# Kernel tuning notes

Hardware: AMD Instinct MI355X
Metric: run time of the kernel (lower is better)

Reference implementation:

```python
import jax, jax.numpy as jnp
import numpy as np

N_NODES = 50000
N_EDGES = 600000
IN_DIM = 128
HID = 128
OUT_DIM = 2
N_GRAPHS = 64
EPS = 1e-12  # F.normalize default eps


def setup_inputs() -> dict:
    key = jax.random.key(0)
    ks = jax.random.split(key, 16)
    s = 0.05
    x = jax.random.normal(ks[0], (N_NODES, IN_DIM), jnp.float32)
    edge_index = jax.random.randint(ks[1], (2, N_EDGES), 0, N_NODES, dtype=jnp.int32)
    batch = jnp.sort(jax.random.randint(ks[2], (N_NODES,), 0, N_GRAPHS, dtype=jnp.int32))
    # GraphSage layer 0: lin (IN->HID), agg_lin (IN+HID -> HID)
    lin_w0 = jax.random.normal(ks[3], (IN_DIM, HID), jnp.float32) * s
    lin_b0 = jnp.zeros((HID,), jnp.float32)
    agg_w0 = jax.random.normal(ks[4], (HID + IN_DIM, HID), jnp.float32) * s
    agg_b0 = jnp.zeros((HID,), jnp.float32)
    # GraphSage layer 1: lin (HID->HID), agg_lin (2*HID -> HID)
    lin_w1 = jax.random.normal(ks[5], (HID, HID), jnp.float32) * s
    lin_b1 = jnp.zeros((HID,), jnp.float32)
    agg_w1 = jax.random.normal(ks[6], (2 * HID, HID), jnp.float32) * s
    agg_b1 = jnp.zeros((HID,), jnp.float32)
    # post_mp: Linear(HID,HID) -> Dropout -> Linear(HID,OUT)
    mp_w1 = jax.random.normal(ks[7], (HID, HID), jnp.float32) * s
    mp_b1 = jnp.zeros((HID,), jnp.float32)
    mp_w2 = jax.random.normal(ks[8], (HID, OUT_DIM), jnp.float32) * s
    mp_b2 = jnp.zeros((OUT_DIM,), jnp.float32)
    return dict(x=x, edge_index=edge_index, batch=batch,
                lin_w0=lin_w0, lin_b0=lin_b0, agg_w0=agg_w0, agg_b0=agg_b0,
                lin_w1=lin_w1, lin_b1=lin_b1, agg_w1=agg_w1, agg_b1=agg_b1,
                mp_w1=mp_w1, mp_b1=mp_b1, mp_w2=mp_w2, mp_b2=mp_b2)


def sage_layer(x, lin_w, lin_b, agg_w, agg_b, src, dst, num_nodes):
    # message: ReLU(Linear(x_j)) gathered along source nodes  [E, HID]
    msg = jax.nn.relu(x[src] @ lin_w + lin_b)
    # aggr='mean' scatter to target nodes
    summed = jax.ops.segment_sum(msg, dst, num_segments=num_nodes)
    deg = jax.ops.segment_sum(jnp.ones((src.shape[0], 1), x.dtype), dst,
                              num_segments=num_nodes)
    agg = summed / jnp.maximum(deg, 1.0)
    # update: ReLU(Linear([aggr, x])) then L2-normalize rows
    h = jax.nn.relu(jnp.concatenate([agg, x], axis=-1) @ agg_w + agg_b)
    norm = jnp.sqrt(jnp.sum(h * h, axis=1, keepdims=True))
    return h / jnp.maximum(norm, EPS)


def reference(x, edge_index, batch,
              lin_w0, lin_b0, agg_w0, agg_b0,
              lin_w1, lin_b1, agg_w1, agg_b1,
              mp_w1, mp_b1, mp_w2, mp_b2):
    src, dst = edge_index[0], edge_index[1]
    n = x.shape[0]
    h = sage_layer(x, lin_w0, lin_b0, agg_w0, agg_b0, src, dst, n)
    # F.relu is a no-op on the non-negative normalized output; dropout p=0 -> identity
    h = sage_layer(h, lin_w1, lin_b1, agg_w1, agg_b1, src, dst, n)
    # global max pool over graphs
    pooled = jax.ops.segment_max(h, batch, num_segments=N_GRAPHS)
    pooled = jnp.where(jnp.isfinite(pooled), pooled, 0.0)  # guard empty graphs
    # post_mp: Linear -> Dropout(identity) -> Linear
    z = (pooled @ mp_w1 + mp_b1) @ mp_w2 + mp_b2
    return jax.nn.log_softmax(z, axis=1)
```

## Files before the change

### kernel.cpp

```cpp
#include <hip/hip_runtime.h>

__device__ __forceinline__ float bf2f(ushort u) {
    union { uint i; float f; } c; c.i = ((uint)u) << 16; return c.f;
}
__device__ __forceinline__ float bf2lo(uint v) {
    union { uint i; float f; } c; c.i = v << 16; return c.f;
}
__device__ __forceinline__ float bf2hi(uint v) {
    union { uint i; float f; } c; c.i = v & 0xffff0000u; return c.f;
}
__device__ __forceinline__ ushort f2bf(float f) {
    union { float f; uint i; } c; c.f = f;
    uint b = c.i;
    uint r = (b + 0x7fffu + ((b >> 16) & 1u)) >> 16;
    return (ushort)r;
}

typedef __bf16 v8bf __attribute__((ext_vector_type(8)));
typedef float  v4f  __attribute__((ext_vector_type(4)));

__device__ __forceinline__ ushort load_conv(const void* src, int i, int isf32) {
    return isf32 ? f2bf(((const float*)src)[i]) : ((const ushort*)src)[i];
}

struct SmallSrcs { const void* p[8]; };
__global__ __launch_bounds__(256) void phaseA(
    const void* __restrict__ x, ushort* __restrict__ xb, int nx, int nbconv,
    const void* __restrict__ w0, const void* __restrict__ wa0,
    const void* __restrict__ w1, const void* __restrict__ wa1,
    ushort* __restrict__ t0, ushort* __restrict__ ta0,
    ushort* __restrict__ t1, ushort* __restrict__ ta1,
    SmallSrcs s, ushort* __restrict__ smalldst,
    int* __restrict__ deg, int* __restrict__ pooled, int N, int G,
    int* __restrict__ flagOut) {
    __shared__ int sred[256];
    int b = blockIdx.x, t = threadIdx.x;
    {
        const uint* words = (const uint*)x;
        int bad = 0;
        for (int i = t; i < 2048; i += 256) {
            uint w = words[i];
            uint exp = (w >> 7) & 0xffu;
            if (exp >= 143u) bad++;
        }
        sred[t] = bad;
        __syncthreads();
        for (int o = 128; o; o >>= 1) {
            if (t < o) sred[t] += sred[t + o];
            __syncthreads();
        }
    }
    const int isf = sred[0] > 64 ? 1 : 0;
    if (b == 0 && t == 0) *flagOut = isf;

    if (b < nbconv) {
        int idx = b * 256 + t;
        int base = idx * 8;
        if (base + 8 <= nx) {
            if (isf) {
                const float4* s4 = (const float4*)x;
                float4 a = s4[idx * 2], bb = s4[idx * 2 + 1];
                union { ushort u[8]; uint4 v; } o;
                o.u[0] = f2bf(a.x); o.u[1] = f2bf(a.y); o.u[2] = f2bf(a.z); o.u[3] = f2bf(a.w);
                o.u[4] = f2bf(bb.x); o.u[5] = f2bf(bb.y); o.u[6] = f2bf(bb.z); o.u[7] = f2bf(bb.w);
                *(uint4*)(xb + base) = o.v;
            } else {
                *(uint4*)(xb + base) = ((const uint4*)x)[idx];
            }
        } else {
            for (int i = base; i < nx; i++) xb[i] = load_conv(x, i, isf);
        }
    } else if (b < nbconv + 452) {
        int idx = (b - nbconv) * 256 + t;
        if (idx < 98304) {
            const void* W; ushort* T; int K; int local;
            if (idx < 16384)      { W = w0;  T = t0;  K = 128; local = idx; }
            else if (idx < 49152) { W = wa0; T = ta0; K = 256; local = idx - 16384; }
            else if (idx < 65536) { W = w1;  T = t1;  K = 128; local = idx - 49152; }
            else                  { W = wa1; T = ta1; K = 256; local = idx - 65536; }
            ushort v = load_conv(W, local, isf);
            int k = local >> 7;
            int n = local & 127;
            T[(size_t)n * K + k] = v;
        } else {
            int si = idx - 98304;
            if (si < 17282) {
                const int offs[9] = {0, 128, 256, 384, 512, 16896, 17024, 17280, 17282};
                int seg = 0;
                while (si >= offs[seg + 1]) seg++;
                smalldst[si] = load_conv(s.p[seg], si - offs[seg], isf);
            }
        }
    } else {
        int idx = (b - nbconv - 452) * 256 + t;
        int nd4 = N >> 2;
        int4 z = {0, 0, 0, 0};
        if (idx < nd4) ((int4*)deg)[idx] = z;
        else if (idx == nd4) { for (int i = nd4 * 4; i < N; i++) deg[i] = 0; }
        else if (idx - nd4 - 1 < G * 32) ((int4*)pooled)[idx - nd4 - 1] = z;
    }
}

__global__ __launch_bounds__(256) void count_deg(const int* __restrict__ dst, int* __restrict__ deg, int E) {
    int i = blockIdx.x * 256 + threadIdx.x;
    if (i < E) atomicAdd(&deg[dst[i]], 1);
}

#define SCAN_CHUNK 1024

__global__ __launch_bounds__(256) void chunk_sum_kernel(const int* __restrict__ deg,
                                                        int* __restrict__ csums, int n) {
    __shared__ int s[256];
    int t = threadIdx.x;
    int base = blockIdx.x * SCAN_CHUNK + t * 4;
    int v = 0;
    if (base + 4 <= n) {
        int4 q = *(const int4*)(deg + base);
        v = q.x + q.y + q.z + q.w;
    } else {
        for (int i = base; i < n; i++) v += deg[i];
    }
    s[t] = v;
    __syncthreads();
    for (int o = 128; o; o >>= 1) {
        if (t < o) s[t] += s[t + o];
        __syncthreads();
    }
    if (t == 0) csums[blockIdx.x] = s[0];
}

__global__ __launch_bounds__(256) void scan_phase2(const int* __restrict__ deg,
                                                   const int* __restrict__ csums,
                                                   int* __restrict__ rowptr, int* __restrict__ cursor,
                                                   int n) {
    __shared__ int red[256];
    int t = threadIdx.x, b = blockIdx.x;
    int v = 0;
    for (int i = t; i < b; i += 256) v += csums[i];
    red[t] = v;
    __syncthreads();
    for (int o = 128; o; o >>= 1) {
        if (t < o) red[t] += red[t + o];
        __syncthreads();
    }
    int chunkOff = red[0];
    __syncthreads();
    int base = b * SCAN_CHUNK + t * 4;
    int d0 = 0, d1 = 0, d2 = 0, d3 = 0;
    if (base + 4 <= n) {
        int4 q = *(const int4*)(deg + base);
        d0 = q.x; d1 = q.y; d2 = q.z; d3 = q.w;
    } else {
        if (base < n)     d0 = deg[base];
        if (base + 1 < n) d1 = deg[base + 1];
        if (base + 2 < n) d2 = deg[base + 2];
        if (base + 3 < n) d3 = deg[base + 3];
    }
    int s4 = d0 + d1 + d2 + d3;
    red[t] = s4;
    __syncthreads();
    for (int o = 1; o < 256; o <<= 1) {
        int u = (t >= o) ? red[t - o] : 0;
        __syncthreads();
        red[t] += u;
        __syncthreads();
    }
    int run = chunkOff + red[t] - s4;
    if (base < n)     { rowptr[base]     = run; cursor[base]     = run; run += d0; }
    if (base + 1 < n) { rowptr[base + 1] = run; cursor[base + 1] = run; run += d1; }
    if (base + 2 < n) { rowptr[base + 2] = run; cursor[base + 2] = run; run += d2; }
    if (base + 3 < n) { rowptr[base + 3] = run; cursor[base + 3] = run; run += d3; }
    if (n >= base && n < base + 4) rowptr[n] = run;
}

__global__ __launch_bounds__(256) void fill_kernel(const int* __restrict__ src, const int* __restrict__ dst,
                                                   int* __restrict__ cursor, int* __restrict__ csr_src, int E) {
    int i = blockIdx.x * 256 + threadIdx.x;
    if (i < E) {
        int pos = atomicAdd(&cursor[dst[i]], 1);
        csr_src[pos] = src[i];
    }
}

template <int NSTAGE, bool NORM, bool POOL, bool FUSE>
__global__ __launch_bounds__(256) void gemm_kernel(
    const ushort* __restrict__ A0, const ushort* __restrict__ A1,
    const ushort* __restrict__ Bt, const ushort* __restrict__ bias,
    ushort* __restrict__ Cout, int M,
    const int* __restrict__ batchv, int* __restrict__ pooled,
    const ushort* __restrict__ Bt2, const ushort* __restrict__ bias2,
    ushort* __restrict__ Mout) {
    __shared__ __bf16 AsT[128 * 136];
    __shared__ __bf16 BsT[128 * 136];
    __shared__ int PoolLoc[POOL ? 8 * 128 : 1];
    const int t = threadIdx.x;
    const int w = t >> 6, lane = t & 63, ln = lane & 15, q = lane >> 4;
    const int blockRow = blockIdx.x * 128;
    const int K = NSTAGE * 128;

    if (POOL) {
        for (int i = t; i < 8 * 128; i += 256) PoolLoc[i] = 0;
    }

    v4f acc[2][8];
#pragma unroll
    for (int i = 0; i < 2; i++)
#pragma unroll
        for (int j = 0; j < 8; j++) acc[i][j] = (v4f){0.f, 0.f, 0.f, 0.f};

#pragma unroll
    for (int st = 0; st < NSTAGE; st++) {
        const ushort* Ap = st ? A1 : A0;
#pragma unroll
        for (int i = 0; i < 8; i++) {
            int c = i * 256 + t;
            int row = c >> 4, k8 = (c & 15) * 8;
            int grow = blockRow + row; if (grow >= M) grow = M - 1;
            *(uint4*)&AsT[row * 136 + k8] = *(const uint4*)(Ap + (size_t)grow * 128 + k8);
            *(uint4*)&BsT[row * 136 + k8] = *(const uint4*)(Bt + (size_t)row * K + st * 128 + k8);
        }
        __syncthreads();
#pragma unroll
        for (int k0 = 0; k0 < 128; k0 += 32) {
            v8bf a0 = *(const v8bf*)&AsT[(w * 32 + ln) * 136 + k0 + q * 8];
            v8bf a1 = *(const v8bf*)&AsT[(w * 32 + 16 + ln) * 136 + k0 + q * 8];
#pragma unroll
            for (int nt = 0; nt < 8; nt++) {
                v8bf b = *(const v8bf*)&BsT[(nt * 16 + ln) * 136 + k0 + q * 8];
                acc[0][nt] = __builtin_amdgcn_mfma_f32_16x16x32_bf16(a0, b, acc[0][nt], 0, 0, 0);
                acc[1][nt] = __builtin_amdgcn_mfma_f32_16x16x32_bf16(a1, b, acc[1][nt], 0, 0, 0);
            }
        }
        __syncthreads();
    }

    float biasf[8];
#pragma unroll
    for (int nt = 0; nt < 8; nt++) biasf[nt] = bf2f(bias[nt * 16 + ln]);

    const int minB = POOL ? batchv[blockRow < M ? blockRow : M - 1] : 0;
    ushort* HsU = (ushort*)AsT;

#pragma unroll
    for (int mt = 0; mt < 2; mt++) {
        float v[8][4];
#pragma unroll
        for (int nt = 0; nt < 8; nt++)
#pragma unroll
            for (int r = 0; r < 4; r++) {
                float x = acc[mt][nt][r] + biasf[nt];
                v[nt][r] = x > 0.f ? x : 0.f;
            }
        float inv[4];
        if (NORM) {
#pragma unroll
            for (int r = 0; r < 4; r++) {
                float p = 0.f;
#pragma unroll
                for (int nt = 0; nt < 8; nt++) p += v[nt][r] * v[nt][r];
                p += __shfl_xor(p, 1);
                p += __shfl_xor(p, 2);
                p += __shfl_xor(p, 4);
                p += __shfl_xor(p, 8);
                inv[r] = 1.0f / fmaxf(sqrtf(p), 1e-12f);
            }
        }
        int rowloc = w * 32 + mt * 16 + q * 4;
#pragma unroll
        for (int r = 0; r < 4; r++) {
            int grow = blockRow + rowloc + r;
            if (POOL) {
                if (grow < M) {
                    int b = batchv[grow];
                    int rel = b - minB;
#pragma unroll
                    for (int nt = 0; nt < 8; nt++) {
                        float x = v[nt][r] * inv[r];
                        int xi = __float_as_int(x);
                        if (rel < 8) atomicMax(&PoolLoc[rel * 128 + nt * 16 + ln], xi);
                        else         atomicMax(&pooled[b * 128 + nt * 16 + ln], xi);
                    }
                }
            } else {
#pragma unroll
                for (int nt = 0; nt < 8; nt++) {
                    float x = NORM ? v[nt][r] * inv[r] : v[nt][r];
                    ushort xb = f2bf(x);
                    if (grow < M) Cout[(size_t)grow * 128 + nt * 16 + ln] = xb;
                    if (FUSE) HsU[(rowloc + r) * 136 + nt * 16 + ln] = xb;
                }
            }
        }
    }

    if (POOL) {
        __syncthreads();
        int lastRow = blockRow + 127; if (lastRow >= M) lastRow = M - 1;
        int span = batchv[lastRow] - minB + 1;
        if (span > 8) span = 8;
        for (int i = t; i < span * 128; i += 256) {
            int vv = PoolLoc[i];
            if (vv != 0) atomicMax(&pooled[(minB + (i >> 7)) * 128 + (i & 127)], vv);
        }
    }

    if (FUSE) {
#pragma unroll
        for (int i = 0; i < 8; i++) {
            int c = i * 256 + t;
            int row = c >> 4, k8 = (c & 15) * 8;
            *(uint4*)&BsT[row * 136 + k8] = *(const uint4*)(Bt2 + (size_t)row * 128 + k8);
        }
        __syncthreads();

        v4f acc2[2][8];
#pragma unroll
        for (int i = 0; i < 2; i++)
#pragma unroll
            for (int j = 0; j < 8; j++) acc2[i][j] = (v4f){0.f, 0.f, 0.f, 0.f};

#pragma unroll
        for (int k0 = 0; k0 < 128; k0 += 32) {
            v8bf a0 = *(const v8bf*)&AsT[(w * 32 + ln) * 136 + k0 + q * 8];
            v8bf a1 = *(const v8bf*)&AsT[(w * 32 + 16 + ln) * 136 + k0 + q * 8];
#pragma unroll
            for (int nt = 0; nt < 8; nt++) {
                v8bf b = *(const v8bf*)&BsT[(nt * 16 + ln) * 136 + k0 + q * 8];
                acc2[0][nt] = __builtin_amdgcn_mfma_f32_16x16x32_bf16(a0, b, acc2[0][nt], 0, 0, 0);
                acc2[1][nt] = __builtin_amdgcn_mfma_f32_16x16x32_bf16(a1, b, acc2[1][nt], 0, 0, 0);
            }
        }

        float biasf2[8];
#pragma unroll
        for (int nt = 0; nt < 8; nt++) biasf2[nt] = bf2f(bias2[nt * 16 + ln]);
#pragma unroll
        for (int mt = 0; mt < 2; mt++) {
            int rowbase = blockRow + w * 32 + mt * 16 + q * 4;
#pragma unroll
            for (int r = 0; r < 4; r++) {
                int grow = rowbase + r;
                if (grow < M) {
#pragma unroll
                    for (int nt = 0; nt < 8; nt++) {
                        float x = acc2[mt][nt][r] + biasf2[nt];
                        Mout[(size_t)grow * 128 + nt * 16 + ln] = f2bf(x > 0.f ? x : 0.f);
                    }
                }
            }
        }
    }
}

__global__ __launch_bounds__(256) void aggregate_kernel(
    const ushort* __restrict__ msg, const int* __restrict__ rowptr,
    const int* __restrict__ csr_src, ushort* __restrict__ agg, int n) {
    int wid = (int)((blockIdx.x * 256u + threadIdx.x) >> 6);
    int lane = threadIdx.x & 63;
    int sub = lane >> 4;
    int l16 = lane & 15;
    if (wid >= n) return;
    int start = rowptr[wid], end = rowptr[wid + 1];
    float a[8] = {0.f, 0.f, 0.f, 0.f, 0.f, 0.f, 0.f, 0.f};
#pragma unroll 2
    for (int j = start + sub; j < end; j += 4) {
        int s = csr_src[j];
        uint4 v = *(const uint4*)(msg + (size_t)s * 128 + l16 * 8);
        a[0] += bf2lo(v.x); a[1] += bf2hi(v.x);
        a[2] += bf2lo(v.y); a[3] += bf2hi(v.y);
        a[4] += bf2lo(v.z); a[5] += bf2hi(v.z);
        a[6] += bf2lo(v.w); a[7] += bf2hi(v.w);
    }
#pragma unroll
    for (int i = 0; i < 8; i++) {
        a[i] += __shfl_xor(a[i], 16);
        a[i] += __shfl_xor(a[i], 32);
    }
    if (sub == 0) {
        float inv = 1.0f / fmaxf((float)(end - start), 1.0f);
        union { ushort u[8]; uint4 v; } o;
#pragma unroll
        for (int i = 0; i < 8; i++) o.u[i] = f2bf(a[i] * inv);
        *(uint4*)(agg + (size_t)wid * 128 + l16 * 8) = o.v;
    }
}

__global__ __launch_bounds__(256) void final_kernel(const float* __restrict__ pooled,
                                                    const ushort* __restrict__ small,
                                                    void* __restrict__ out, int G,
                                                    const int* __restrict__ flag) {
    __shared__ float P[128];
    __shared__ float Thalf[128];
    __shared__ float T[128];
    __shared__ float R0[128], R1[128];
    const ushort* w1 = small + 512;
    const ushort* b1 = small + 16896;
    const ushort* w2 = small + 17024;
    const ushort* b2 = small + 17280;
    int g = blockIdx.x;
    int t = threadIdx.x;
    int j = t & 127, half = t >> 7;
    if (t < 128) P[t] = pooled[g * 128 + t];
    __syncthreads();
    float acc = 0.f;
    int k0 = half * 64;
#pragma unroll 8
    for (int k = k0; k < k0 + 64; k++) acc += P[k] * bf2f(w1[k * 128 + j]);
    if (half == 0) Thalf[j] = acc;
    __syncthreads();
    if (half == 1) T[j] = Thalf[j] + acc + bf2f(b1[j]);
    __syncthreads();
    if (t < 128) {
        float tv = T[t];
        R0[t] = tv * bf2f(w2[t * 2]);
        R1[t] = tv * bf2f(w2[t * 2 + 1]);
    }
    __syncthreads();
    for (int o = 64; o; o >>= 1) {
        if (t < o) { R0[t] += R0[t + o]; R1[t] += R1[t + o]; }
        __syncthreads();
    }
    if (t == 0) {
        float z0 = R0[0] + bf2f(b2[0]);
        float z1 = R1[0] + bf2f(b2[1]);
        float m = fmaxf(z0, z1);
        float l = m + logf(expf(z0 - m) + expf(z1 - m));
        float o0 = z0 - l, o1 = z1 - l;
        if (*flag) {
            ((float*)out)[2 * g]     = o0;
            ((float*)out)[2 * g + 1] = o1;
        } else {
            ((ushort*)out)[2 * g]     = f2bf(o0);
            ((ushort*)out)[2 * g + 1] = f2bf(o1);
        }
    }
}

extern "C" void kernel_launch(void* const* d_in, const int* in_sizes, int n_in,
                              void* d_out, int out_size, void* d_ws, size_t ws_size,
                              hipStream_t stream) {
    const void* x      = d_in[0];
    const int*  ei     = (const int*)d_in[1];
    const int*  batch  = (const int*)d_in[2];

    const int N = in_sizes[0] / 128;
    const int E = in_sizes[1] / 2;
    const int G = out_size / 2;
    const int* srcIdx = ei;
    const int* dstIdx = ei + E;

    char* ws = (char*)d_ws;
    size_t off = 0;
    auto alloc = [&](size_t bytes) -> void* {
        off = (off + 255) & ~(size_t)255;
        void* p = ws + off;
        off += bytes;
        return p;
    };
    int*    flag    = (int*)alloc(4);
    int*    deg     = (int*)alloc((size_t)N * 4);
    int*    rowptr  = (int*)alloc((size_t)(N + 1) * 4);
    int*    cursor  = (int*)alloc((size_t)N * 4);
    int*    csr_src = (int*)alloc((size_t)E * 4);
    int*    csums   = (int*)alloc(((size_t)N / SCAN_CHUNK + 2) * 4);
    ushort* Wt0     = (ushort*)alloc(128 * 128 * 2);
    ushort* WtA0    = (ushort*)alloc(256 * 128 * 2);
    ushort* Wt1     = (ushort*)alloc(128 * 128 * 2);
    ushort* WtA1    = (ushort*)alloc(256 * 128 * 2);
    ushort* small   = (ushort*)alloc(17282 * 2);
    ushort* xb      = (ushort*)alloc((size_t)N * 128 * 2);
    ushort* msg     = (ushort*)alloc((size_t)N * 128 * 2);
    ushort* agg     = (ushort*)alloc((size_t)N * 128 * 2);
    ushort* h0      = (ushort*)alloc((size_t)N * 128 * 2);
    int*    pooled  = (int*)alloc((size_t)G * 128 * 4);

    SmallSrcs ss;
    ss.p[0] = d_in[4];  ss.p[1] = d_in[6];  ss.p[2] = d_in[8];  ss.p[3] = d_in[10];
    ss.p[4] = d_in[11]; ss.p[5] = d_in[12]; ss.p[6] = d_in[13]; ss.p[7] = d_in[14];
    int nbconv = (N * 128 + 2047) / 2048;
    int nbzero = ((N / 4 + 1 + G * 32) + 255) / 256;
    phaseA<<<nbconv + 452 + nbzero, 256, 0, stream>>>(
        x, xb, N * 128, nbconv,
        d_in[3], d_in[5], d_in[7], d_in[9],
        Wt0, WtA0, Wt1, WtA1, ss, small, deg, pooled, N, G, flag);

    int gb = (N + 127) / 128;
    int ab = (N + 3) / 4;
    int eb = (E + 255) / 256;

    gemm_kernel<1, false, false, false><<<gb, 256, 0, stream>>>(
        xb, xb, Wt0, small + 0, msg, N, nullptr, nullptr, nullptr, nullptr, nullptr);

    count_deg<<<eb, 256, 0, stream>>>(dstIdx, deg, E);
    int nchunks = (N + SCAN_CHUNK - 1) / SCAN_CHUNK;
    chunk_sum_kernel<<<nchunks, 256, 0, stream>>>(deg, csums, N);
    scan_phase2<<<N / SCAN_CHUNK + 1, 256, 0, stream>>>(deg, csums, rowptr, cursor, N);
    fill_kernel<<<eb, 256, 0, stream>>>(srcIdx, dstIdx, cursor, csr_src, E);

    aggregate_kernel<<<ab, 256, 0, stream>>>(msg, rowptr, csr_src, agg, N);
    gemm_kernel<2, true, false, true><<<gb, 256, 0, stream>>>(
        agg, xb, WtA0, small + 128, h0, N, nullptr, nullptr, Wt1, small + 256, msg);

    aggregate_kernel<<<ab, 256, 0, stream>>>(msg, rowptr, csr_src, agg, N);
    gemm_kernel<2, true, true, false><<<gb, 256, 0, stream>>>(
        agg, h0, WtA1, small + 384, nullptr, N, batch, pooled, nullptr, nullptr, nullptr);

    final_kernel<<<G, 256, 0, stream>>>((const float*)pooled, small, d_out, G, flag);
}
```

Baseline: 274.2 us.

## Fuse neighbor mean aggregation into the update GEMM A-tile load

Removes the separate aggregate kernels and has the update GEMM gather and mean-reduce neighbor messages straight into its shared-memory A tile. Two message buffers are ping-ponged so the fused layer-0 kernel can write layer-1 messages while reading layer-0 ones. This avoids writing and re-reading the agg array and saves two launches. In exchange, a 16-thread group now walks one node's edge list serially with no cross-group parallelism, while a 256-thread GEMM block with large LDS use is held during the irregular gather, which may lower occupancy and memory-level parallelism.

```diff
diff --git a/kernel.cpp b/kernel.cpp
--- a/kernel.cpp
+++ b/kernel.cpp
@@ -182,14 +182,16 @@
     }
 }
 
-template <int NSTAGE, bool NORM, bool POOL, bool FUSE>
+template <int NSTAGE, bool NORM, bool POOL, bool FUSE, bool AGG>
 __global__ __launch_bounds__(256) void gemm_kernel(
     const ushort* __restrict__ A0, const ushort* __restrict__ A1,
     const ushort* __restrict__ Bt, const ushort* __restrict__ bias,
     ushort* __restrict__ Cout, int M,
     const int* __restrict__ batchv, int* __restrict__ pooled,
     const ushort* __restrict__ Bt2, const ushort* __restrict__ bias2,
-    ushort* __restrict__ Mout) {
+    ushort* __restrict__ Mout,
+    const int* __restrict__ rowptr, const int* __restrict__ csr_src,
+    const ushort* __restrict__ msgsrc) {
     __shared__ __bf16 AsT[128 * 136];
     __shared__ __bf16 BsT[128 * 136];
     __shared__ int PoolLoc[POOL ? 8 * 128 : 1];
@@ -210,14 +212,44 @@
 
 #pragma unroll
     for (int st = 0; st < NSTAGE; st++) {
-        const ushort* Ap = st ? A1 : A0;
 #pragma unroll
         for (int i = 0; i < 8; i++) {
             int c = i * 256 + t;
             int row = c >> 4, k8 = (c & 15) * 8;
-            int grow = blockRow + row; if (grow >= M) grow = M - 1;
-            *(uint4*)&AsT[row * 136 + k8] = *(const uint4*)(Ap + (size_t)grow * 128 + k8);
             *(uint4*)&BsT[row * 136 + k8] = *(const uint4*)(Bt + (size_t)row * K + st * 128 + k8);
+        }
+        if (AGG && st == 0) {
+            int grp = t >> 4, l16 = t & 15;
+#pragma unroll
+            for (int pass = 0; pass < 8; pass++) {
+                int nn = pass * 16 + grp;
+                int node = blockRow + nn; if (node >= M) node = M - 1;
+                int start = rowptr[node], end = rowptr[node + 1];
+                float a[8] = {0.f, 0.f, 0.f, 0.f, 0.f, 0.f, 0.f, 0.f};
+#pragma unroll 4
+                for (int j = start; j < end; j++) {
+                    int s = csr_src[j];
+                    uint4 v = *(const uint4*)(msgsrc + (size_t)s * 128 + l16 * 8);
+                    a[0] += bf2lo(v.x); a[1] += bf2hi(v.x);
+                    a[2] += bf2lo(v.y); a[3] += bf2hi(v.y);
+                    a[4] += bf2lo(v.z); a[5] += bf2hi(v.z);
+                    a[6] += bf2lo(v.w); a[7] += bf2hi(v.w);
+                }
+                float inv = 1.0f / fmaxf((float)(end - start), 1.0f);
+                union { ushort u[8]; uint4 v; } o;
+#pragma unroll
+                for (int i = 0; i < 8; i++) o.u[i] = f2bf(a[i] * inv);
+                *(uint4*)&AsT[nn * 136 + l16 * 8] = o.v;
+            }
+        } else {
+            const ushort* Ap = st ? A1 : A0;
+#pragma unroll
+            for (int i = 0; i < 8; i++) {
+                int c = i * 256 + t;
+                int row = c >> 4, k8 = (c & 15) * 8;
+                int grow = blockRow + row; if (grow >= M) grow = M - 1;
+                *(uint4*)&AsT[row * 136 + k8] = *(const uint4*)(Ap + (size_t)grow * 128 + k8);
+            }
         }
         __syncthreads();
 #pragma unroll
@@ -349,39 +381,6 @@
                 }
             }
         }
-    }
-}
-
-__global__ __launch_bounds__(256) void aggregate_kernel(
-    const ushort* __restrict__ msg, const int* __restrict__ rowptr,
-    const int* __restrict__ csr_src, ushort* __restrict__ agg, int n) {
-    int wid = (int)((blockIdx.x * 256u + threadIdx.x) >> 6);
-    int lane = threadIdx.x & 63;
-    int sub = lane >> 4;
-    int l16 = lane & 15;
-    if (wid >= n) return;
-    int start = rowptr[wid], end = rowptr[wid + 1];
-    float a[8] = {0.f, 0.f, 0.f, 0.f, 0.f, 0.f, 0.f, 0.f};
-#pragma unroll 2
-    for (int j = start + sub; j < end; j += 4) {
-        int s = csr_src[j];
-        uint4 v = *(const uint4*)(msg + (size_t)s * 128 + l16 * 8);
-        a[0] += bf2lo(v.x); a[1] += bf2hi(v.x);
-        a[2] += bf2lo(v.y); a[3] += bf2hi(v.y);
-        a[4] += bf2lo(v.z); a[5] += bf2hi(v.z);
-        a[6] += bf2lo(v.w); a[7] += bf2hi(v.w);
-    }
-#pragma unroll
-    for (int i = 0; i < 8; i++) {
-        a[i] += __shfl_xor(a[i], 16);
-        a[i] += __shfl_xor(a[i], 32);
-    }
-    if (sub == 0) {
-        float inv = 1.0f / fmaxf((float)(end - start), 1.0f);
-        union { ushort u[8]; uint4 v; } o;
-#pragma unroll
-        for (int i = 0; i < 8; i++) o.u[i] = f2bf(a[i] * inv);
-        *(uint4*)(agg + (size_t)wid * 128 + l16 * 8) = o.v;
     }
 }
 
@@ -469,8 +468,8 @@
     ushort* WtA1    = (ushort*)alloc(256 * 128 * 2);
     ushort* small   = (ushort*)alloc(17282 * 2);
     ushort* xb      = (ushort*)alloc((size_t)N * 128 * 2);
-    ushort* msg     = (ushort*)alloc((size_t)N * 128 * 2);
-    ushort* agg     = (ushort*)alloc((size_t)N * 128 * 2);
+    ushort* msgA    = (ushort*)alloc((size_t)N * 128 * 2);
+    ushort* msgB    = (ushort*)alloc((size_t)N * 128 * 2);
     ushort* h0      = (ushort*)alloc((size_t)N * 128 * 2);
     int*    pooled  = (int*)alloc((size_t)G * 128 * 4);
 
@@ -485,11 +484,11 @@
         Wt0, WtA0, Wt1, WtA1, ss, small, deg, pooled, N, G, flag);
 
     int gb = (N + 127) / 128;
-    int ab = (N + 3) / 4;
     int eb = (E + 255) / 256;
 
-    gemm_kernel<1, false, false, false><<<gb, 256, 0, stream>>>(
-        xb, xb, Wt0, small + 0, msg, N, nullptr, nullptr, nullptr, nullptr, nullptr);
+    gemm_kernel<1, false, false, false, false><<<gb, 256, 0, stream>>>(
+        xb, xb, Wt0, small + 0, msgA, N, nullptr, nullptr, nullptr, nullptr, nullptr,
+        nullptr, nullptr, nullptr);
 
     count_deg<<<eb, 256, 0, stream>>>(dstIdx, deg, E);
     int nchunks = (N + SCAN_CHUNK - 1) / SCAN_CHUNK;
@@ -497,13 +496,13 @@
     scan_phase2<<<N / SCAN_CHUNK + 1, 256, 0, stream>>>(deg, csums, rowptr, cursor, N);
     fill_kernel<<<eb, 256, 0, stream>>>(srcIdx, dstIdx, cursor, csr_src, E);
 
-    aggregate_kernel<<<ab, 256, 0, stream>>>(msg, rowptr, csr_src, agg, N);
-    gemm_kernel<2, true, false, true><<<gb, 256, 0, stream>>>(
-        agg, xb, WtA0, small + 128, h0, N, nullptr, nullptr, Wt1, small + 256, msg);
-
-    aggregate_kernel<<<ab, 256, 0, stream>>>(msg, rowptr, csr_src, agg, N);
-    gemm_kernel<2, true, true, false><<<gb, 256, 0, stream>>>(
-        agg, h0, WtA1, small + 384, nullptr, N, batch, pooled, nullptr, nullptr, nullptr);
+    gemm_kernel<2, true, false, true, true><<<gb, 256, 0, stream>>>(
+        nullptr, xb, WtA0, small + 128, h0, N, nullptr, nullptr, Wt1, small + 256, msgB,
+        rowptr, csr_src, msgA);
+
+    gemm_kernel<2, true, true, false, true><<<gb, 256, 0, stream>>>(
+        nullptr, h0, WtA1, small + 384, nullptr, N, batch, pooled, nullptr, nullptr, nullptr,
+        rowptr, csr_src, msgB);
 
     final_kernel<<<G, 256, 0, stream>>>((const float*)pooled, small, d_out, G, flag);
 }
```

Result: slower. 288.9 us (+5.4%).
